# Optimization experiments

Measured on AMD Instinct MI355X. Metric: run time of the kernel, lower is better.

Reference implementation:

```python
import jax, jax.numpy as jnp
import numpy as np

B, I, M, R, C = 2048, 16, 4, 4096, 10  # batch, input_dim, num_mfs, num_rules, num_classes


def setup_inputs() -> dict:
    key = jax.random.key(0)
    k1, k2, k3, k4, k5 = jax.random.split(key, 5)
    x = jax.random.normal(k1, (B, I), dtype=jnp.float32)
    centers = jax.random.normal(k2, (I, M), dtype=jnp.float32)
    widths = jax.random.uniform(k3, (I, M), dtype=jnp.float32, minval=0.5, maxval=1.5)
    consequents = jax.random.normal(k4, (R, I + 1, C), dtype=jnp.float32)
    rule_idx = jax.random.randint(k5, (I, R), 0, M, dtype=jnp.int32)
    return {"x": x, "centers": centers, "widths": widths,
            "consequents": consequents, "rule_idx": rule_idx}


def reference(x, centers, widths, consequents, rule_idx):
    # Gaussian membership functions: [B, I, M] (note: +1e-9 inside exp, as in source)
    mfs = jnp.exp(-(x[:, :, None] - centers[None]) ** 2 / (2.0 * widths[None] ** 2) + 1e-9)
    # Gather per-rule MF values along the M axis: [B, I, R]
    rule_mfs = mfs[:, jnp.arange(I)[:, None], rule_idx]
    # Product t-norm over input dims -> firing strengths [B, R]
    firing = jnp.prod(rule_mfs, axis=1)
    norm_fs = firing / (jnp.sum(firing, axis=1, keepdims=True) + 1e-9)
    # Extended input with bias [B, I+1]
    x_ext = jnp.concatenate([x, jnp.ones((x.shape[0], 1), dtype=x.dtype)], axis=1)
    # Outer product phi [B, R, I+1], then flat GEMM with consequents
    phi = norm_fs[:, :, None] * jax.lax.stop_gradient(x_ext)[:, None, :]
    y_hat = phi.reshape(x.shape[0], R * (I + 1)) @ consequents.reshape(R * (I + 1), C)
    return y_hat, norm_fs, x_ext
```

## Files before the change

### kernel.cpp

```cpp
#include <hip/hip_runtime.h>
#include <stdint.h>

typedef short short8 __attribute__((ext_vector_type(8)));
typedef float f32x4 __attribute__((ext_vector_type(4)));

#define B_ 2048
#define I_ 16
#define M_ 4
#define R_ 4096
#define C_ 10
#define NX 17
#define NW 170
#define NPAD 192
#define KSPLIT 32
#define KCH (R_ / KSPLIT)
#define NIT (KCH / 32)

#define Y_OFF    0
#define NORM_OFF (B_ * C_)
#define XE_OFF   (B_ * C_ + B_ * R_)

#define PK_OFF    0
#define WT_OFF    16384
#define NFB_OFF   (WT_OFF + NPAD * R_ * 2)
#define PARTY_OFF (NFB_OFF + B_ * R_ * 2)

#define MFMA16(a, b, c) __builtin_amdgcn_mfma_f32_16x16x32_bf16(a, b, c, 0, 0, 0)

__device__ __forceinline__ uint16_t f2bf(float f) {
    uint32_t u = __builtin_bit_cast(uint32_t, f);
    uint32_t r = u + 0x7fffu + ((u >> 16) & 1u);
    return (uint16_t)(r >> 16);
}

__global__ __launch_bounds__(256) void prep_kernel(
        const int* __restrict__ rule_idx, const float* __restrict__ cons,
        uint32_t* __restrict__ packed, uint16_t* __restrict__ wt) {
    int t = threadIdx.x;
    if (blockIdx.x == 64) {
        for (int r = t; r < R_; r += 256) {
            uint32_t p = 0;
#pragma unroll
            for (int i = 0; i < I_; ++i)
                p |= ((uint32_t)rule_idx[i * R_ + r] & 3u) << (2 * i);
            packed[r] = p;
        }
        return;
    }
    __shared__ float lt[64][NW + 1];
    int k0 = blockIdx.x * 64;
    for (int idx = t; idx < 64 * NW; idx += 256) {
        int k = idx / NW, n = idx - k * NW;
        lt[k][n] = cons[(size_t)(k0 + k) * NW + n];
    }
    __syncthreads();
    for (int idx = t; idx < NPAD * 32; idx += 256) {
        int n = idx >> 5, kp = idx & 31;
        uint32_t v = 0;
        if (n < NW) {
            uint32_t v0 = f2bf(lt[kp * 2][n]);
            uint32_t v1 = f2bf(lt[kp * 2 + 1][n]);
            v = v0 | (v1 << 16);
        }
        *(uint32_t*)(wt + (size_t)n * R_ + k0 + kp * 2) = v;
    }
}

__global__ __launch_bounds__(256) void fuzz_kernel(
        const float* __restrict__ x, const float* __restrict__ centers,
        const float* __restrict__ widths, const uint32_t* __restrict__ packed,
        float* __restrict__ out, uint16_t* __restrict__ nfb) {
    int b = blockIdx.x;
    int t = threadIdx.x;
    __shared__ float xs[I_];
    __shared__ float zl[64];
    __shared__ float tab4[4 * 256];
    __shared__ float wsum[4];

    if (t < I_) xs[t] = x[b * I_ + t];
    if (t < NX) out[XE_OFF + b * NX + t] = (t < I_) ? x[b * I_ + t] : 1.0f;
    __syncthreads();

    if (t < 64) {
        int i = t >> 2, m = t & 3;
        float d = xs[i] - centers[i * M_ + m];
        float w = widths[i * M_ + m];
        zl[t] = -(d * d) / (2.0f * w * w) + 1e-9f;
    }
    __syncthreads();

#pragma unroll
    for (int u = 0; u < 4; ++u) {
        int idx = t + u * 256;
        int q = idx >> 8, xq = idx & 255;
        tab4[idx] = zl[q * 16 +      (xq & 3)]
                  + zl[q * 16 +  4 + ((xq >> 2) & 3)]
                  + zl[q * 16 +  8 + ((xq >> 4) & 3)]
                  + zl[q * 16 + 12 + ((xq >> 6) & 3)];
    }
    __syncthreads();

    uint2 pk[8];
#pragma unroll
    for (int k = 0; k < 8; ++k)
        pk[k] = *(const uint2*)(packed + t * 2 + k * 512);

    float fs[16];
    float lsum = 0.f;
#pragma unroll
    for (int k = 0; k < 8; ++k) {
#pragma unroll
        for (int j = 0; j < 2; ++j) {
            uint32_t p = j ? pk[k].y : pk[k].x;
            float s = tab4[        p         & 255]
                    + tab4[256 + ((p >>  8) & 255)]
                    + tab4[512 + ((p >> 16) & 255)]
                    + tab4[768 + ((p >> 24) & 255)];
            float f = __expf(s);
            fs[k * 2 + j] = f;
            lsum += f;
        }
    }
#pragma unroll
    for (int off = 32; off > 0; off >>= 1) lsum += __shfl_down(lsum, off);
    if ((t & 63) == 0) wsum[t >> 6] = lsum;
    __syncthreads();
    float inv = 1.0f / (wsum[0] + wsum[1] + wsum[2] + wsum[3] + 1e-9f);

    float* orow = out + NORM_OFF + (size_t)b * R_ + t * 2;
    uint16_t* nrow = nfb + (size_t)b * R_ + t * 2;
#pragma unroll
    for (int k = 0; k < 8; ++k) {
        float n0 = fs[k * 2] * inv;
        float n1 = fs[k * 2 + 1] * inv;
        *(float2*)(orow + k * 512) = make_float2(n0, n1);
        uint32_t pkd = (uint32_t)f2bf(n0) | ((uint32_t)f2bf(n1) << 16);
        *(uint32_t*)(nrow + k * 512) = pkd;
    }
}

__global__ __launch_bounds__(256, 3) void gemm_kernel(
        const uint16_t* __restrict__ nfb,
        const uint16_t* __restrict__ wt,
        const float* __restrict__ xe,
        float* __restrict__ party) {
    int bt  = blockIdx.x;
    int ks  = blockIdx.y;
    int tid = threadIdx.x;
    int wid = tid >> 6;
    int lane = tid & 63;
    int b0 = bt * 64;
    int k0 = ks * KCH;
    int row = lane & 15;
    int kf  = (lane >> 4) * 8;

    f32x4 acc[4][3];
#pragma unroll
    for (int mt = 0; mt < 4; ++mt)
#pragma unroll
        for (int nt = 0; nt < 3; ++nt) acc[mt][nt] = (f32x4){0.f, 0.f, 0.f, 0.f};

    const uint16_t* Ab = nfb + (size_t)(b0 + row) * R_ + k0 + kf;
    const uint16_t* Bb = wt  + (size_t)(wid * 48 + row) * R_ + k0 + kf;

    short8 a[2][4], w[2][3];
#define LOADS(buf, kk)                                                   \
    do {                                                                 \
        a[buf][0] = *(const short8*)(Ab + (kk));                         \
        a[buf][1] = *(const short8*)(Ab + (size_t)16 * R_ + (kk));       \
        a[buf][2] = *(const short8*)(Ab + (size_t)32 * R_ + (kk));       \
        a[buf][3] = *(const short8*)(Ab + (size_t)48 * R_ + (kk));       \
        w[buf][0] = *(const short8*)(Bb + (kk));                         \
        w[buf][1] = *(const short8*)(Bb + (size_t)16 * R_ + (kk));       \
        w[buf][2] = *(const short8*)(Bb + (size_t)32 * R_ + (kk));       \
    } while (0)

    LOADS(0, 0);
#pragma unroll
    for (int it = 0; it < NIT; ++it) {
        int cur = it & 1;
        if (it + 1 < NIT) LOADS(cur ^ 1, (it + 1) * 32);
#pragma unroll
        for (int nt = 0; nt < 3; ++nt)
#pragma unroll
            for (int mt = 0; mt < 4; ++mt)
                acc[mt][nt] = MFMA16(a[cur][mt], w[cur][nt], acc[mt][nt]);
    }
#undef LOADS

    __shared__ float tile[64][NPAD];
#pragma unroll
    for (int mt = 0; mt < 4; ++mt)
#pragma unroll
        for (int nt = 0; nt < 3; ++nt)
#pragma unroll
            for (int j = 0; j < 4; ++j)
                tile[mt * 16 + (lane >> 4) * 4 + j][wid * 48 + nt * 16 + row] =
                    acc[mt][nt][j];
    __syncthreads();

    for (int idx = tid; idx < 64 * C_; idx += 256) {
        int bl = idx / C_;
        int c  = idx - bl * C_;
        float y = tile[bl][I_ * C_ + c];
        const float* xrow = xe + (size_t)(b0 + bl) * NX;
#pragma unroll
        for (int j = 0; j < I_; ++j) y += xrow[j] * tile[bl][j * C_ + c];
        party[((size_t)ks * B_ + b0 + bl) * C_ + c] = y;
    }
}

__global__ __launch_bounds__(256) void finalize_kernel(
        const float* __restrict__ party, float* __restrict__ out) {
    int idx = blockIdx.x * 256 + threadIdx.x;
    if (idx < B_ * C_) {
        float s = 0.f;
#pragma unroll
        for (int ks = 0; ks < KSPLIT; ++ks) s += party[(size_t)ks * B_ * C_ + idx];
        out[Y_OFF + idx] = s;
    }
}

extern "C" void kernel_launch(void* const* d_in, const int* in_sizes, int n_in,
                              void* d_out, int out_size, void* d_ws, size_t ws_size,
                              hipStream_t stream) {
    const float* x       = (const float*)d_in[0];
    const float* centers = (const float*)d_in[1];
    const float* widths  = (const float*)d_in[2];
    const float* cons    = (const float*)d_in[3];
    const int*   ridx    = (const int*)d_in[4];
    float* out = (float*)d_out;

    uint32_t* packed = (uint32_t*)((char*)d_ws + PK_OFF);
    uint16_t* wt     = (uint16_t*)((char*)d_ws + WT_OFF);
    uint16_t* nfb    = (uint16_t*)((char*)d_ws + NFB_OFF);
    float*    party  = (float*)((char*)d_ws + PARTY_OFF);

    prep_kernel<<<dim3(65), dim3(256), 0, stream>>>(ridx, cons, packed, wt);
    fuzz_kernel<<<dim3(B_), dim3(256), 0, stream>>>(x, centers, widths, packed, out, nfb);
    gemm_kernel<<<dim3(B_ / 64, KSPLIT), dim3(256), 0, stream>>>(
        nfb, wt, out + XE_OFF, party);
    finalize_kernel<<<dim3((B_ * C_ + 255) / 256), dim3(256), 0, stream>>>(party, out);
}
```

Before: 47.15 us.

## Fuse weight transpose into fuzz kernel, replace split-K finalize with atomics

Spreads rule-index packing across 16 blocks that also zero the output y, folds the consequent transpose/bf16 conversion into the fuzzification launch as 64 extra blocks, and removes the finalize kernel by having GEMM blocks atomically add their split-K partials into y. The norm_fs output store becomes nontemporal. The aim is to cut two kernel launches, the serial single-block packing work and the partial-sum buffer round trip, at the cost of 32-way float atomic contention per output element and nondeterministic summation order.

```diff
diff --git a/kernel.cpp b/kernel.cpp
--- a/kernel.cpp
+++ b/kernel.cpp
@@ -3,6 +3,7 @@
 
 typedef short short8 __attribute__((ext_vector_type(8)));
 typedef float f32x4 __attribute__((ext_vector_type(4)));
+typedef float f32x2 __attribute__((ext_vector_type(2)));
 
 #define B_ 2048
 #define I_ 16
@@ -22,8 +23,6 @@
 
 #define PK_OFF    0
 #define WT_OFF    16384
-#define NFB_OFF   (WT_OFF + NPAD * R_ * 2)
-#define PARTY_OFF (NFB_OFF + B_ * R_ * 2)
 
 #define MFMA16(a, b, c) __builtin_amdgcn_mfma_f32_16x16x32_bf16(a, b, c, 0, 0, 0)
 
@@ -33,49 +32,61 @@
     return (uint16_t)(r >> 16);
 }
 
-__global__ __launch_bounds__(256) void prep_kernel(
-        const int* __restrict__ rule_idx, const float* __restrict__ cons,
-        uint32_t* __restrict__ packed, uint16_t* __restrict__ wt) {
+__global__ __launch_bounds__(256) void pack_kernel(
+        const int* __restrict__ rule_idx, uint32_t* __restrict__ packed,
+        float* __restrict__ out) {
     int t = threadIdx.x;
-    if (blockIdx.x == 64) {
-        for (int r = t; r < R_; r += 256) {
-            uint32_t p = 0;
-#pragma unroll
-            for (int i = 0; i < I_; ++i)
-                p |= ((uint32_t)rule_idx[i * R_ + r] & 3u) << (2 * i);
-            packed[r] = p;
+    int r = blockIdx.x * 256 + t;
+    uint32_t p = 0;
+#pragma unroll
+    for (int i = 0; i < I_; ++i)
+        p |= ((uint32_t)rule_idx[i * R_ + r] & 3u) << (2 * i);
+    packed[r] = p;
+    f32x4* y4 = (f32x4*)(out + Y_OFF);
+    int base = (blockIdx.x * 256 + t) * 5;
+#pragma unroll
+    for (int u = 0; u < 5; ++u) y4[base + u] = (f32x4){0.f, 0.f, 0.f, 0.f};
+}
+
+__global__ __launch_bounds__(256) void fuzz_wt_kernel(
+        const float* __restrict__ x, const float* __restrict__ centers,
+        const float* __restrict__ widths, const uint32_t* __restrict__ packed,
+        const float* __restrict__ cons, float* __restrict__ out,
+        uint16_t* __restrict__ nfb, uint16_t* __restrict__ wt) {
+    __shared__ float smem[16 * (NW + 2)];
+    int t = threadIdx.x;
+
+    if (blockIdx.x >= B_) {
+        int k0 = (blockIdx.x - B_) * 64;
+        float (*lt)[NW + 2] = (float (*)[NW + 2])smem;
+#pragma unroll
+        for (int tile = 0; tile < 4; ++tile) {
+            int kt0 = k0 + tile * 16;
+            for (int idx = t; idx < 16 * NW; idx += 256) {
+                int k = idx / NW, n = idx - k * NW;
+                lt[k][n] = cons[(size_t)(kt0 + k) * NW + n];
+            }
+            __syncthreads();
+            for (int idx = t; idx < NPAD * 8; idx += 256) {
+                int n = idx >> 3, kp = idx & 7;
+                uint32_t v = 0;
+                if (n < NW) {
+                    uint32_t v0 = f2bf(lt[kp * 2][n]);
+                    uint32_t v1 = f2bf(lt[kp * 2 + 1][n]);
+                    v = v0 | (v1 << 16);
+                }
+                *(uint32_t*)(wt + (size_t)n * R_ + kt0 + kp * 2) = v;
+            }
+            __syncthreads();
         }
         return;
     }
-    __shared__ float lt[64][NW + 1];
-    int k0 = blockIdx.x * 64;
-    for (int idx = t; idx < 64 * NW; idx += 256) {
-        int k = idx / NW, n = idx - k * NW;
-        lt[k][n] = cons[(size_t)(k0 + k) * NW + n];
-    }
-    __syncthreads();
-    for (int idx = t; idx < NPAD * 32; idx += 256) {
-        int n = idx >> 5, kp = idx & 31;
-        uint32_t v = 0;
-        if (n < NW) {
-            uint32_t v0 = f2bf(lt[kp * 2][n]);
-            uint32_t v1 = f2bf(lt[kp * 2 + 1][n]);
-            v = v0 | (v1 << 16);
-        }
-        *(uint32_t*)(wt + (size_t)n * R_ + k0 + kp * 2) = v;
-    }
-}
-
-__global__ __launch_bounds__(256) void fuzz_kernel(
-        const float* __restrict__ x, const float* __restrict__ centers,
-        const float* __restrict__ widths, const uint32_t* __restrict__ packed,
-        float* __restrict__ out, uint16_t* __restrict__ nfb) {
+
     int b = blockIdx.x;
-    int t = threadIdx.x;
-    __shared__ float xs[I_];
-    __shared__ float zl[64];
-    __shared__ float tab4[4 * 256];
-    __shared__ float wsum[4];
+    float* xs   = smem;
+    float* zl   = smem + 16;
+    float* tab4 = smem + 80;
+    float* wsum = smem + 1104;
 
     if (t < I_) xs[t] = x[b * I_ + t];
     if (t < NX) out[XE_OFF + b * NX + t] = (t < I_) ? x[b * I_ + t] : 1.0f;
@@ -133,7 +144,8 @@
     for (int k = 0; k < 8; ++k) {
         float n0 = fs[k * 2] * inv;
         float n1 = fs[k * 2 + 1] * inv;
-        *(float2*)(orow + k * 512) = make_float2(n0, n1);
+        f32x2 o2 = {n0, n1};
+        __builtin_nontemporal_store(o2, (f32x2*)(orow + k * 512));
         uint32_t pkd = (uint32_t)f2bf(n0) | ((uint32_t)f2bf(n1) << 16);
         *(uint32_t*)(nrow + k * 512) = pkd;
     }
@@ -143,7 +155,7 @@
         const uint16_t* __restrict__ nfb,
         const uint16_t* __restrict__ wt,
         const float* __restrict__ xe,
-        float* __restrict__ party) {
+        float* __restrict__ out) {
     int bt  = blockIdx.x;
     int ks  = blockIdx.y;
     int tid = threadIdx.x;
@@ -206,18 +218,7 @@
         const float* xrow = xe + (size_t)(b0 + bl) * NX;
 #pragma unroll
         for (int j = 0; j < I_; ++j) y += xrow[j] * tile[bl][j * C_ + c];
-        party[((size_t)ks * B_ + b0 + bl) * C_ + c] = y;
-    }
-}
-
-__global__ __launch_bounds__(256) void finalize_kernel(
-        const float* __restrict__ party, float* __restrict__ out) {
-    int idx = blockIdx.x * 256 + threadIdx.x;
-    if (idx < B_ * C_) {
-        float s = 0.f;
-#pragma unroll
-        for (int ks = 0; ks < KSPLIT; ++ks) s += party[(size_t)ks * B_ * C_ + idx];
-        out[Y_OFF + idx] = s;
+        atomicAdd(&out[Y_OFF + (size_t)(b0 + bl) * C_ + c], y);
     }
 }
 
@@ -233,12 +234,11 @@
 
     uint32_t* packed = (uint32_t*)((char*)d_ws + PK_OFF);
     uint16_t* wt     = (uint16_t*)((char*)d_ws + WT_OFF);
-    uint16_t* nfb    = (uint16_t*)((char*)d_ws + NFB_OFF);
-    float*    party  = (float*)((char*)d_ws + PARTY_OFF);
-
-    prep_kernel<<<dim3(65), dim3(256), 0, stream>>>(ridx, cons, packed, wt);
-    fuzz_kernel<<<dim3(B_), dim3(256), 0, stream>>>(x, centers, widths, packed, out, nfb);
+    uint16_t* nfb    = (uint16_t*)((char*)d_ws + WT_OFF + NPAD * R_ * 2);
+
+    pack_kernel<<<dim3(R_ / 256), dim3(256), 0, stream>>>(ridx, packed, out);
+    fuzz_wt_kernel<<<dim3(B_ + 64), dim3(256), 0, stream>>>(
+        x, centers, widths, packed, cons, out, nfb, wt);
     gemm_kernel<<<dim3(B_ / 64, KSPLIT), dim3(256), 0, stream>>>(
-        nfb, wt, out + XE_OFF, party);
-    finalize_kernel<<<dim3((B_ * C_ + 255) / 256), dim3(256), 0, stream>>>(party, out);
-}
+        nfb, wt, out + XE_OFF, out);
+}
```

New measurement: 54.92 us. 1.16x slower.
